# Performance work log

Measured on AMD Instinct MI355X. Metric: run time of the kernel, lower is better.

Reference implementation:

```python
import jax, jax.numpy as jnp
import numpy as np

B, L, D_MODEL, D_INNER, P = 4, 16384, 256, 512, 64  # P = d_state, conj_sym=False
STEP_RESCALE = 1.0


def setup_inputs() -> dict:
    key = jax.random.key(0)
    ks = jax.random.split(key, 11)
    # projections (bias=False)
    W_in = jax.random.normal(ks[0], (D_MODEL, 2 * D_INNER), jnp.float32) * (1.0 / np.sqrt(D_MODEL))
    W_out = jax.random.normal(ks[1], (D_INNER, D_MODEL), jnp.float32) * (1.0 / np.sqrt(D_INNER))
    # diagonal SSM params: Lambda = A_real + i*A_imag, HiPPO-like (negative real part)
    A_real = -0.5 * jnp.ones((P,), jnp.float32) - jax.random.uniform(ks[2], (P,), jnp.float32)
    A_imag = jnp.pi * jnp.arange(P, dtype=jnp.float32) * (jax.random.uniform(ks[3], (P,), jnp.float32) * 0.1 + 0.95)
    B_re = jax.random.normal(ks[4], (P, D_INNER), jnp.float32) * (1.0 / np.sqrt(P))
    B_im = jax.random.normal(ks[5], (P, D_INNER), jnp.float32) * (1.0 / np.sqrt(P))
    C_re = jax.random.normal(ks[6], (D_INNER, P), jnp.float32) * (1.0 / np.sqrt(D_INNER))
    C_im = jax.random.normal(ks[7], (D_INNER, P), jnp.float32) * (1.0 / np.sqrt(D_INNER))
    D = jax.random.normal(ks[8], (D_INNER,), jnp.float32)
    # dt ~ loguniform[dt_min, dt_max]; inv_dt = softplus^{-1}(dt) = dt + log(-expm1(-dt))
    dt = jnp.exp(jax.random.uniform(ks[9], (P,), jnp.float32) * (np.log(0.1) - np.log(0.001)) + np.log(0.001))
    dt = jnp.clip(dt, 1e-4, None)
    inv_dt = dt + jnp.log(-jnp.expm1(-dt))
    x = jax.random.normal(ks[10], (B, L, D_MODEL), jnp.float32)
    return {"x": x, "W_in": W_in, "W_out": W_out, "A_real": A_real, "A_imag": A_imag,
            "B_re": B_re, "B_im": B_im, "C_re": C_re, "C_im": C_im, "D": D, "inv_dt": inv_dt}


def _binop(e1, e2):
    a1, b1 = e1
    a2, b2 = e2
    return a2 * a1, a2 * b1 + b2


def reference(x, W_in, W_out, A_real, A_imag, B_re, B_im, C_re, C_im, D, inv_dt):
    # in_proj + gate split
    x_and_res = x @ W_in                       # (b, l, 2*d_inner)
    u, res = jnp.split(x_and_res, 2, axis=-1)
    u = jax.nn.silu(u)                         # (b, l, d_inner)
    # bilinear discretization of diagonal SSM
    A = A_real + 1j * A_imag                   # (P,)
    dt = STEP_RESCALE * jax.nn.softplus(inv_dt)  # (P,)
    BL = 1.0 / (1.0 - (dt / 2.0) * A)
    dA = BL * (1.0 + (dt / 2.0) * A)           # (P,)
    dB = (BL * dt)[:, None] * (B_re + 1j * B_im)  # (P, d_inner)
    # drive: Bu_t = dB @ u_t
    Bu = u.astype(dA.dtype) @ dB.T             # (b, l, P) complex
    # parallel (associative) scan of h_t = dA*h_{t-1} + Bu_t  (h_0 = 0)
    elems = (jnp.broadcast_to(dA, Bu.shape), Bu)
    _, h = jax.lax.associative_scan(_binop, elems, axis=1)  # (b, l, P)
    C = C_re + 1j * C_im                       # (d_inner, P)
    y = jnp.real(h @ C.T) + D * u              # (b, l, d_inner), + skip D*u
    y = y * jax.nn.silu(res)
    return y @ W_out                           # (b, l, d_model)
```

## Files before the change

kernel.cpp:

```cpp
#include <hip/hip_runtime.h>
#include <math.h>

#define NTOK 65536
#define LSEQ 16384
#define GCH 64
#define NCH 256

typedef __attribute__((ext_vector_type(8))) short short8v;
typedef __attribute__((ext_vector_type(4))) float f32x4;
typedef unsigned short u16;

__device__ __forceinline__ u16 f2bf(float f) {
  unsigned u = __float_as_uint(f);
  return (u16)((u + 0x7FFFu + ((u >> 16) & 1u)) >> 16);
}
__device__ __forceinline__ float bf2f(u16 b) {
  return __uint_as_float(((unsigned)b) << 16);
}
__device__ __forceinline__ unsigned cvtpk_bf16(float lo, float hi) {
  unsigned r;
  asm("v_cvt_pk_bf16_f32 %0, %1, %2" : "=v"(r) : "v"(lo), "v"(hi));
  return r;
}
__device__ __forceinline__ float silu_f(float v) {
  return v * __builtin_amdgcn_rcpf(1.f + __expf(-v));
}
__device__ __forceinline__ void gld16(const u16* g, u16* l) {
  __builtin_amdgcn_global_load_lds((const __attribute__((address_space(1))) void*)g,
                                   (__attribute__((address_space(3))) void*)l, 16, 0, 0);
}

#define GLOAD(dst, ptr) \
  asm volatile("global_load_dwordx4 %0, %1, off" : "=&v"(dst) : "v"(ptr) : "memory")
#define SCHEDB __builtin_amdgcn_sched_barrier(0)
#define WAITV4 asm volatile("s_waitcnt vmcnt(4)" ::: "memory")
#define WAITV1a asm volatile("s_waitcnt vmcnt(1)" ::: "memory")
#define WAITV3L asm volatile("s_waitcnt vmcnt(3) lgkmcnt(0)" ::: "memory")
#define WAITV2 asm volatile("s_waitcnt vmcnt(2) lgkmcnt(0)" ::: "memory")
#define WAITV1 asm volatile("s_waitcnt vmcnt(1) lgkmcnt(0)" ::: "memory")
#define WAITV0 asm volatile("s_waitcnt vmcnt(0) lgkmcnt(0)" ::: "memory")
#define BARRAW asm volatile("s_barrier" ::: "memory")

__global__ void setup_scalar_k(const float* __restrict__ A_real, const float* __restrict__ A_imag,
                               const float* __restrict__ inv_dt,
                               float2* __restrict__ dAf, float2* __restrict__ fvec,
                               float2* __restrict__ powt) {
  int p = threadIdx.x;
  if (p >= 64) return;
  double ar = (double)A_real[p], ai = (double)A_imag[p];
  double dt = log1p(exp((double)inv_dt[p]));
  double zr = 0.5 * dt * ar, zi = 0.5 * dt * ai;
  double d1r = 1.0 - zr;
  double den = d1r * d1r + zi * zi;
  double blr = d1r / den, bli = zi / den;
  double nr = 1.0 + zr, ni = zi;
  double dar = blr * nr - bli * ni;
  double dai = blr * ni + bli * nr;
  dAf[p] = make_float2((float)dar, (float)dai);
  fvec[p] = make_float2((float)(blr * dt), (float)(bli * dt));
  double cr = 1.0, ci = 0.0;
  for (int k = 0; k <= GCH; ++k) {
    powt[p * (GCH + 1) + k] = make_float2((float)cr, (float)ci);
    double t = cr * dar - ci * dai;
    ci = cr * dai + ci * dar;
    cr = t;
  }
}

__global__ void setup_tables_k(const float* __restrict__ B_re, const float* __restrict__ B_im,
                               const float* __restrict__ C_re, const float* __restrict__ C_im,
                               const float* __restrict__ W_in, const float* __restrict__ W_out,
                               const float2* __restrict__ fvec,
                               u16* __restrict__ WinT, u16* __restrict__ dBn,
                               u16* __restrict__ Ccb, u16* __restrict__ WoutT) {
  int idx = blockIdx.x * blockDim.x + threadIdx.x;
  int stride = gridDim.x * blockDim.x;
  for (int i = idx; i < 1024 * 256; i += stride) {
    int n = i >> 8, k = i & 255;
    WinT[i] = f2bf(W_in[k * 1024 + n]);
  }
  for (int i = idx; i < 128 * 512; i += stride) {
    int p = i >> 9, d = i & 511;
    float2 f = fvec[p & 63];
    float br = B_re[(p & 63) * 512 + d], bi = B_im[(p & 63) * 512 + d];
    float v = (p < 64) ? (f.x * br - f.y * bi) : (f.x * bi + f.y * br);
    dBn[i] = f2bf(v);
  }
  for (int i = idx; i < 512 * 128; i += stride) {
    int d = i >> 7, k = i & 127;
    float v = (k < 64) ? C_re[d * 64 + k] : -C_im[d * 64 + (k - 64)];
    Ccb[i] = f2bf(v);
  }
  for (int i = idx; i < 256 * 512; i += stride) {
    int n = i >> 9, k = i & 511;
    WoutT[i] = f2bf(W_out[k * 256 + n]);
  }
}

__global__ __launch_bounds__(512) void k1_fused(
    const float* __restrict__ X, const u16* __restrict__ WinT,
    u16* __restrict__ u_bf, u16* __restrict__ sr_bf) {
  constexpr int KDIM = 256, NT = 8;
  __shared__ u16 As[2][128 * 32];
  __shared__ u16 Bs[3][128 * 32];
  const int tid = threadIdx.x;
  const int w = tid >> 6, l = tid & 63;
  const int wm = w >> 2, wn = w & 3;

  const int lin = blockIdx.x;
  const int cpx = gridDim.x >> 3;
  const int swz = (lin & 7) * cpx + (lin >> 3);
  const int n0 = (swz & 7) * 128;
  const int m0 = (swz >> 3) * 128;

  f32x4 acc[4][2] = {};
  const int fr = l & 15;
  const int kgs = (((l >> 4) ^ (l >> 1)) & 3) * 8;
  const int sr = l >> 2;
  const int scl = l & 3;
  const int scs = scl ^ ((l >> 3) & 3);
  const int arow = w * 16 + sr;
  const float* gA = X + (size_t)(m0 + arow) * KDIM + scl * 8;
  const u16* gB = WinT + (size_t)(n0 + w * 16 + sr) * KDIM + scs * 8;

  float4 rp0, rp1, rq0, rq1;

  auto writeA = [&](int buf, const float4& a0, const float4& a1) {
    unsigned q0 = cvtpk_bf16(a0.x, a0.y), q1 = cvtpk_bf16(a0.z, a0.w);
    unsigned q2 = cvtpk_bf16(a1.x, a1.y), q3 = cvtpk_bf16(a1.z, a1.w);
    *(uint4*)&As[buf][arow * 32 + scs * 8] = make_uint4(q0, q1, q2, q3);
  };
  auto stageB = [&](int buf, int t) { gld16(gB + t * 32, &Bs[buf][w * 512]); };
  auto compute = [&](int ab, int bb) {
    short8v af[4], bfr[2];
#pragma unroll
    for (int mi = 0; mi < 4; ++mi)
      af[mi] = *(const short8v*)&As[ab][(wm * 64 + mi * 16 + fr) * 32 + kgs];
#pragma unroll
    for (int ni = 0; ni < 2; ++ni)
      bfr[ni] = *(const short8v*)&Bs[bb][(wn * 32 + ni * 16 + fr) * 32 + kgs];
#pragma unroll
    for (int mi = 0; mi < 4; ++mi)
#pragma unroll
      for (int ni = 0; ni < 2; ++ni)
        acc[mi][ni] = __builtin_amdgcn_mfma_f32_16x16x32_bf16(af[mi], bfr[ni], acc[mi][ni], 0, 0, 0);
  };

  GLOAD(rp0, gA);          GLOAD(rp1, gA + 4);
  stageB(0, 0);
  GLOAD(rq0, gA + 32);     GLOAD(rq1, gA + 36);
  stageB(1, 1);
  WAITV4; SCHEDB;
  writeA(0, rp0, rp1);
  WAITV3L;
  BARRAW;

#pragma unroll
  for (int t = 0; t < NT; ++t) {
    if (t + 2 < NT) {
      if ((t & 1) == 0) { GLOAD(rp0, gA + (t + 2) * 32); GLOAD(rp1, gA + (t + 2) * 32 + 4); }
      else              { GLOAD(rq0, gA + (t + 2) * 32); GLOAD(rq1, gA + (t + 2) * 32 + 4); }
      stageB((t + 2) % 3, t + 2);
    }
    compute(t & 1, t % 3);
    if (t + 1 < NT) {
      if (t + 2 < NT) { WAITV4; } else { WAITV1a; }
      SCHEDB;
      if (((t + 1) & 1) == 0) writeA(0, rp0, rp1);
      else                    writeA(1, rq0, rq1);
      if (t + 2 < NT) { WAITV3L; } else { WAITV0; }
      BARRAW;
    }
  }

  const int rbase = (l >> 4) * 4;
#pragma unroll
  for (int mi = 0; mi < 4; ++mi) {
#pragma unroll
    for (int ni = 0; ni < 2; ++ni) {
      int gr0 = m0 + wm * 64 + mi * 16 + rbase;
      int gc = n0 + wn * 32 + ni * 16 + fr;
      float s0 = silu_f(acc[mi][ni][0]);
      float s1 = silu_f(acc[mi][ni][1]);
      float s2 = silu_f(acc[mi][ni][2]);
      float s3 = silu_f(acc[mi][ni][3]);
      unsigned p01 = cvtpk_bf16(s0, s1);
      unsigned p23 = cvtpk_bf16(s2, s3);
      u16* Cw = (n0 < 512) ? u_bf : sr_bf;
      int col = gc - ((n0 < 512) ? 0 : 512);
      Cw[(size_t)(gr0 + 0) * 512 + col] = (u16)p01;
      Cw[(size_t)(gr0 + 1) * 512 + col] = (u16)(p01 >> 16);
      Cw[(size_t)(gr0 + 2) * 512 + col] = (u16)p23;
      Cw[(size_t)(gr0 + 3) * 512 + col] = (u16)(p23 >> 16);
    }
  }
}

template<int MODE, int LOG_NBX, int KDIM>
__global__ __launch_bounds__(1024) void mgemm2(
    const u16* __restrict__ Ain, const u16* __restrict__ Bt,
    void* __restrict__ C0, void* __restrict__ C1,
    const float* __restrict__ Dvec) {
  constexpr int NT = KDIM / 32;
  __shared__ u16 As[3][128 * 32];
  __shared__ u16 Bs[3][256 * 32];
  const int tid = threadIdx.x;
  const int w = tid >> 6, l = tid & 63;
  const int wm = w >> 3, wn = w & 7;
  const bool isA = (w < 8);

  const int lin = blockIdx.x;
  const int cpx = gridDim.x >> 3;
  const int swz = (lin & 7) * cpx + (lin >> 3);
  const int n0 = (swz & ((1 << LOG_NBX) - 1)) * 256;
  const int m0 = (swz >> LOG_NBX) * 128;

  f32x4 acc[4][2] = {};

  const int fr = l & 15;
  const int kgs = (((l >> 4) ^ (l >> 1)) & 3) * 8;
  const int sr = l >> 2;
  const int scs = (l & 3) ^ ((l >> 3) & 3);

  const u16* gA = nullptr;
  const u16* gB = nullptr;
  if (isA) gA = Ain + (size_t)(m0 + w * 16 + sr) * KDIM + scs * 8;
  else     gB = Bt + (size_t)(n0 + (w - 8) * 16 + sr) * KDIM + scs * 8;

  auto stage = [&](int buf, int k0) {
    if (isA) {
      gld16(gA + k0, &As[buf][w * 512]);
    } else {
      gld16(gB + k0, &Bs[buf][(w - 8) * 512]);
      gld16(gB + k0 + (size_t)128 * KDIM, &Bs[buf][(w - 8) * 512 + 4096]);
    }
  };
  auto compute = [&](int buf) {
    short8v af[4], bfr[2];
#pragma unroll
    for (int mi = 0; mi < 4; ++mi)
      af[mi] = *(const short8v*)&As[buf][(wm * 64 + mi * 16 + fr) * 32 + kgs];
#pragma unroll
    for (int ni = 0; ni < 2; ++ni)
      bfr[ni] = *(const short8v*)&Bs[buf][(wn * 32 + ni * 16 + fr) * 32 + kgs];
#pragma unroll
    for (int mi = 0; mi < 4; ++mi)
#pragma unroll
      for (int ni = 0; ni < 2; ++ni)
        acc[mi][ni] = __builtin_amdgcn_mfma_f32_16x16x32_bf16(af[mi], bfr[ni], acc[mi][ni], 0, 0, 0);
  };

  stage(0, 0);
  stage(1, 32);
#pragma unroll
  for (int t = 0; t < NT; ++t) {
    if (t + 1 < NT) { if (isA) { WAITV1; } else { WAITV2; } } else { WAITV0; }
    BARRAW;
    if (t + 2 < NT) stage((t + 2) % 3, (t + 2) * 32);
    compute(t % 3);
  }

  const int rbase = (l >> 4) * 4;
#pragma unroll
  for (int mi = 0; mi < 4; ++mi) {
#pragma unroll
    for (int ni = 0; ni < 2; ++ni) {
      int gr0 = m0 + wm * 64 + mi * 16 + rbase;
      int gc = n0 + wn * 32 + ni * 16 + fr;
      if (MODE == 2) {
        float g[4];
#pragma unroll
        for (int j = 0; j < 4; ++j) {
          size_t r = (size_t)(gr0 + j);
          float uu = bf2f(((const u16*)C0)[r * 512 + gc]);
          float sr2 = bf2f(((const u16*)C1)[r * 512 + gc]);
          g[j] = (acc[mi][ni][j] + Dvec[gc] * uu) * sr2;
        }
        unsigned p01 = cvtpk_bf16(g[0], g[1]);
        unsigned p23 = cvtpk_bf16(g[2], g[3]);
        ((u16*)C1)[(size_t)(gr0 + 0) * 512 + gc] = (u16)p01;
        ((u16*)C1)[(size_t)(gr0 + 1) * 512 + gc] = (u16)(p01 >> 16);
        ((u16*)C1)[(size_t)(gr0 + 2) * 512 + gc] = (u16)p23;
        ((u16*)C1)[(size_t)(gr0 + 3) * 512 + gc] = (u16)(p23 >> 16);
      } else {
#pragma unroll
        for (int j = 0; j < 4; ++j)
          ((float*)C0)[(size_t)(gr0 + j) * 256 + gc] = acc[mi][ni][j];
      }
    }
  }
}

__global__ __launch_bounds__(512) void k2_bu_carry(
    const u16* __restrict__ A, const u16* __restrict__ Bt,
    float* __restrict__ Bu, float* __restrict__ carr, float* __restrict__ carr2,
    const float2* __restrict__ dAf, const float2* __restrict__ powt) {
  constexpr int KDIM = 512;
  constexpr int NT = KDIM / 32;
  __shared__ u16 As[3][128 * 32];
  __shared__ u16 Bs[3][128 * 32];
  const int tid = threadIdx.x;
  const int w = tid >> 6, l = tid & 63;
  const int wm = w >> 2, wn = w & 3;

  const int lin = blockIdx.x;
  const int cpx = gridDim.x >> 3;
  const int swz = (lin & 7) * cpx + (lin >> 3);
  const int m0 = swz * 128;

  f32x4 acc[4][2] = {};

  const int lr = l >> 2;
  const int sc = (l & 3) ^ ((l >> 3) & 3);
  const u16* gA = A + (size_t)(m0 + w * 16 + lr) * KDIM + sc * 8;
  const u16* gB = Bt + (size_t)(w * 16 + lr) * KDIM + sc * 8;

  const int fr = l & 15;
  const int kgs = (((l >> 4) ^ (l >> 1)) & 3) * 8;

  auto stage = [&](int buf, int k0) {
    gld16(gA + k0, &As[buf][w * 512]);
    gld16(gB + k0, &Bs[buf][w * 512]);
  };
  auto compute = [&](int buf) {
    short8v af[4], bfr[2];
#pragma unroll
    for (int mi = 0; mi < 4; ++mi)
      af[mi] = *(const short8v*)&As[buf][(wm * 64 + mi * 16 + fr) * 32 + kgs];
#pragma unroll
    for (int ni = 0; ni < 2; ++ni)
      bfr[ni] = *(const short8v*)&Bs[buf][(wn * 32 + ni * 16 + fr) * 32 + kgs];
#pragma unroll
    for (int mi = 0; mi < 4; ++mi)
#pragma unroll
      for (int ni = 0; ni < 2; ++ni)
        acc[mi][ni] = __builtin_amdgcn_mfma_f32_16x16x32_bf16(af[mi], bfr[ni], acc[mi][ni], 0, 0, 0);
  };

  stage(0, 0);
  stage(1, 32);
#pragma unroll
  for (int t = 0; t < NT; ++t) {
    if (t + 1 < NT) { WAITV2; } else { WAITV0; }
    BARRAW;
    if (t + 2 < NT) stage((t + 2) % 3, (t + 2) * 32);
    compute(t % 3);
  }

  const int lg = l >> 4;
  const int rbase = lg * 4;
#pragma unroll
  for (int mi = 0; mi < 4; ++mi)
#pragma unroll
    for (int ni = 0; ni < 2; ++ni) {
      int gr0 = m0 + wm * 64 + mi * 16 + rbase;
      int gc = wn * 32 + ni * 16 + fr;
#pragma unroll
      for (int j = 0; j < 4; ++j)
        Bu[(size_t)(gr0 + j) * 128 + gc] = acc[mi][ni][j];
    }
  const int cu = (m0 >> 6) + wm;
#pragma unroll
  for (int ni = 0; ni < 2; ++ni) {
    int gc = wn * 32 + ni * 16 + fr;
    int p = gc & 63;
    float2 dA = dAf[p];
    float sre = 0.f, sim = 0.f;
#pragma unroll
    for (int mi = 0; mi < 4; ++mi) {
      float tr = 0.f, ti = 0.f;
#pragma unroll
      for (int j = 0; j < 4; ++j) {
        float v = acc[mi][ni][j];
        float nr = fmaf(dA.x, tr, fmaf(-dA.y, ti, v));
        float nim = fmaf(dA.x, ti, dA.y * tr);
        tr = nr; ti = nim;
      }
      float2 wg = powt[p * (GCH + 1) + 60 - lg * 4 - 16 * mi];
      sre = fmaf(wg.x, tr, fmaf(-wg.y, ti, sre));
      sim = fmaf(wg.x, ti, fmaf(wg.y, tr, sim));
    }
    sre += __shfl_xor(sre, 16); sim += __shfl_xor(sim, 16);
    sre += __shfl_xor(sre, 32); sim += __shfl_xor(sim, 32);
    if (lg == 0) {
      size_t crow = (size_t)cu * 128;
      if (gc < 64) { carr[crow + p] = sre;  carr[crow + 64 + p] = sim; }
      else         { carr2[crow + p] = -sim; carr2[crow + 64 + p] = sre; }
    }
  }
}

__global__ void scan_carry_k(const float* __restrict__ carr, const float* __restrict__ carr2,
                             float* __restrict__ offc, const float2* __restrict__ powt) {
  int b = threadIdx.x >> 6;
  int p = threadIdx.x & 63;
  float2 dAG = powt[p * (GCH + 1) + GCH];
  float rr = 0.f, ri = 0.f;
  for (int c0 = 0; c0 < NCH; c0 += 8) {
    float er[8], ei[8];
#pragma unroll
    for (int j = 0; j < 8; ++j) {
      size_t crow = (size_t)(b * NCH + c0 + j) * 128;
      er[j] = carr[crow + p] + carr2[crow + p];
      ei[j] = carr[crow + 64 + p] + carr2[crow + 64 + p];
    }
#pragma unroll
    for (int j = 0; j < 8; ++j) {
      size_t orow = (size_t)(b * NCH + c0 + j) * 128;
      offc[orow + p] = rr;
      offc[orow + 64 + p] = ri;
      float nr = fmaf(dAG.x, rr, fmaf(-dAG.y, ri, er[j]));
      float ni = fmaf(dAG.x, ri, fmaf(dAG.y, rr, ei[j]));
      rr = nr; ri = ni;
    }
  }
}

__global__ __launch_bounds__(256) void scan_emit_k(const float* __restrict__ Bu,
                                                   const float* __restrict__ offc,
                                                   u16* __restrict__ hb,
                                                   const float2* __restrict__ dAf) {
  int unit = blockIdx.x * 4 + (threadIdx.x >> 6);
  int p = threadIdx.x & 63;
  int b = unit >> 8, c = unit & 255;
  float2 dA = dAf[p];
  size_t base = ((size_t)b * LSEQ + (size_t)c * GCH) * 128;
  float hr = offc[(size_t)unit * 128 + p];
  float hi = offc[(size_t)unit * 128 + 64 + p];
  for (int i0 = 0; i0 < GCH; i0 += 8) {
    float br[8], bi[8];
#pragma unroll
    for (int j = 0; j < 8; ++j) {
      br[j] = Bu[base + (size_t)(i0 + j) * 128 + p];
      bi[j] = Bu[base + (size_t)(i0 + j) * 128 + 64 + p];
    }
#pragma unroll
    for (int j = 0; j < 8; ++j) {
      float nr = fmaf(dA.x, hr, fmaf(-dA.y, hi, br[j]));
      float ni = fmaf(dA.x, hi, fmaf(dA.y, hr, bi[j]));
      hr = nr; hi = ni;
      hb[base + (size_t)(i0 + j) * 128 + p] = f2bf(hr);
      hb[base + (size_t)(i0 + j) * 128 + 64 + p] = f2bf(hi);
    }
  }
}

extern "C" void kernel_launch(void* const* d_in, const int* in_sizes, int n_in,
                              void* d_out, int out_size, void* d_ws, size_t ws_size,
                              hipStream_t stream) {
  const float* x      = (const float*)d_in[0];
  const float* W_in   = (const float*)d_in[1];
  const float* W_out  = (const float*)d_in[2];
  const float* A_real = (const float*)d_in[3];
  const float* A_imag = (const float*)d_in[4];
  const float* B_re   = (const float*)d_in[5];
  const float* B_im   = (const float*)d_in[6];
  const float* C_re   = (const float*)d_in[7];
  const float* C_im   = (const float*)d_in[8];
  const float* Dv     = (const float*)d_in[9];
  const float* inv_dt = (const float*)d_in[10];

  u16* u_bf  = (u16*)d_ws;
  u16* sr_bf = u_bf + (size_t)NTOK * 512;
  u16* h_bf  = sr_bf + (size_t)NTOK * 512;
  u16* WinT  = h_bf + (size_t)NTOK * 128;
  u16* dBn   = WinT + 1024 * 256;
  u16* Ccb   = dBn + 128 * 512;
  u16* WoutT = Ccb + 512 * 128;

  float* O    = (float*)d_out;
  float* Bu   = O;
  float* offc = O + 8388608;
  float* carr = O + 8519680;
  float* car2 = O + 8650752;
  float2* powt = (float2*)(O + 8781824);
  float2* dAf  = (float2*)(O + 8790144);
  float2* fvec = (float2*)(O + 8790272);

  setup_scalar_k<<<1, 64, 0, stream>>>(A_real, A_imag, inv_dt, dAf, fvec, powt);
  setup_tables_k<<<256, 256, 0, stream>>>(B_re, B_im, C_re, C_im, W_in, W_out, fvec,
                                          WinT, dBn, Ccb, WoutT);

  k1_fused<<<4096, 512, 0, stream>>>(x, WinT, u_bf, sr_bf);
  k2_bu_carry<<<512, 512, 0, stream>>>(u_bf, dBn, Bu, carr, car2, dAf, powt);
  scan_carry_k<<<1, 256, 0, stream>>>(carr, car2, offc, powt);
  scan_emit_k<<<256, 256, 0, stream>>>(Bu, offc, h_bf, dAf);
  mgemm2<2, 1, 128><<<1024, 1024, 0, stream>>>(h_bf, Ccb, u_bf, sr_bf, Dv);
  mgemm2<3, 0, 512><<<512, 1024, 0, stream>>>(sr_bf, WoutT, O, nullptr, nullptr);
}
```

Before: 223.7 us.

## Pre-convert x to bf16 and stage both GEMM operands via direct LDS loads

Adds a separate pass that converts x to bf16 in workspace, so the in-projection GEMM can load both A and B tiles with global_load_lds into triple-buffered LDS. This replaces the register-staged fp32 loads and in-kernel conversion. The cost is an extra kernel launch plus a write and re-read of a 32 MB bf16 copy of x, traded for a simpler, deeper pipeline. The carry scan kernel also double-buffers its loads, issuing the next 8 chunks before stepping the current ones.

```diff
diff --git a/kernel.cpp b/kernel.cpp
--- a/kernel.cpp
+++ b/kernel.cpp
@@ -30,12 +30,6 @@
                                    (__attribute__((address_space(3))) void*)l, 16, 0, 0);
 }
 
-#define GLOAD(dst, ptr) \
-  asm volatile("global_load_dwordx4 %0, %1, off" : "=&v"(dst) : "v"(ptr) : "memory")
-#define SCHEDB __builtin_amdgcn_sched_barrier(0)
-#define WAITV4 asm volatile("s_waitcnt vmcnt(4)" ::: "memory")
-#define WAITV1a asm volatile("s_waitcnt vmcnt(1)" ::: "memory")
-#define WAITV3L asm volatile("s_waitcnt vmcnt(3) lgkmcnt(0)" ::: "memory")
 #define WAITV2 asm volatile("s_waitcnt vmcnt(2) lgkmcnt(0)" ::: "memory")
 #define WAITV1 asm volatile("s_waitcnt vmcnt(1) lgkmcnt(0)" ::: "memory")
 #define WAITV0 asm volatile("s_waitcnt vmcnt(0) lgkmcnt(0)" ::: "memory")
@@ -97,11 +91,23 @@
   }
 }
 
-__global__ __launch_bounds__(512) void k1_fused(
-    const float* __restrict__ X, const u16* __restrict__ WinT,
+__global__ __launch_bounds__(256) void cvt_x_k(const float* __restrict__ x, u16* __restrict__ xb) {
+  size_t i = ((size_t)blockIdx.x * blockDim.x + threadIdx.x) * 4;
+  size_t stride = (size_t)gridDim.x * blockDim.x * 4;
+  const size_t total = (size_t)NTOK * 256;
+  for (; i < total; i += stride) {
+    float4 v = *(const float4*)(x + i);
+    ushort4 o;
+    o.x = f2bf(v.x); o.y = f2bf(v.y); o.z = f2bf(v.z); o.w = f2bf(v.w);
+    *(ushort4*)(xb + i) = o;
+  }
+}
+
+__global__ __launch_bounds__(512) void k1_gemm(
+    const u16* __restrict__ A, const u16* __restrict__ Bt,
     u16* __restrict__ u_bf, u16* __restrict__ sr_bf) {
   constexpr int KDIM = 256, NT = 8;
-  __shared__ u16 As[2][128 * 32];
+  __shared__ u16 As[3][128 * 32];
   __shared__ u16 Bs[3][128 * 32];
   const int tid = threadIdx.x;
   const int w = tid >> 6, l = tid & 63;
@@ -114,31 +120,27 @@
   const int m0 = (swz >> 3) * 128;
 
   f32x4 acc[4][2] = {};
+
+  const int lr = l >> 2;
+  const int sc = (l & 3) ^ ((l >> 3) & 3);
+  const u16* gA = A + (size_t)(m0 + w * 16 + lr) * KDIM + sc * 8;
+  const u16* gB = Bt + (size_t)(n0 + w * 16 + lr) * KDIM + sc * 8;
+
   const int fr = l & 15;
   const int kgs = (((l >> 4) ^ (l >> 1)) & 3) * 8;
-  const int sr = l >> 2;
-  const int scl = l & 3;
-  const int scs = scl ^ ((l >> 3) & 3);
-  const int arow = w * 16 + sr;
-  const float* gA = X + (size_t)(m0 + arow) * KDIM + scl * 8;
-  const u16* gB = WinT + (size_t)(n0 + w * 16 + sr) * KDIM + scs * 8;
-
-  float4 rp0, rp1, rq0, rq1;
-
-  auto writeA = [&](int buf, const float4& a0, const float4& a1) {
-    unsigned q0 = cvtpk_bf16(a0.x, a0.y), q1 = cvtpk_bf16(a0.z, a0.w);
-    unsigned q2 = cvtpk_bf16(a1.x, a1.y), q3 = cvtpk_bf16(a1.z, a1.w);
-    *(uint4*)&As[buf][arow * 32 + scs * 8] = make_uint4(q0, q1, q2, q3);
-  };
-  auto stageB = [&](int buf, int t) { gld16(gB + t * 32, &Bs[buf][w * 512]); };
-  auto compute = [&](int ab, int bb) {
+
+  auto stage = [&](int buf, int k0) {
+    gld16(gA + k0, &As[buf][w * 512]);
+    gld16(gB + k0, &Bs[buf][w * 512]);
+  };
+  auto compute = [&](int buf) {
     short8v af[4], bfr[2];
 #pragma unroll
     for (int mi = 0; mi < 4; ++mi)
-      af[mi] = *(const short8v*)&As[ab][(wm * 64 + mi * 16 + fr) * 32 + kgs];
+      af[mi] = *(const short8v*)&As[buf][(wm * 64 + mi * 16 + fr) * 32 + kgs];
 #pragma unroll
     for (int ni = 0; ni < 2; ++ni)
-      bfr[ni] = *(const short8v*)&Bs[bb][(wn * 32 + ni * 16 + fr) * 32 + kgs];
+      bfr[ni] = *(const short8v*)&Bs[buf][(wn * 32 + ni * 16 + fr) * 32 + kgs];
 #pragma unroll
     for (int mi = 0; mi < 4; ++mi)
 #pragma unroll
@@ -146,48 +148,31 @@
         acc[mi][ni] = __builtin_amdgcn_mfma_f32_16x16x32_bf16(af[mi], bfr[ni], acc[mi][ni], 0, 0, 0);
   };
 
-  GLOAD(rp0, gA);          GLOAD(rp1, gA + 4);
-  stageB(0, 0);
-  GLOAD(rq0, gA + 32);     GLOAD(rq1, gA + 36);
-  stageB(1, 1);
-  WAITV4; SCHEDB;
-  writeA(0, rp0, rp1);
-  WAITV3L;
-  BARRAW;
-
+  stage(0, 0);
+  stage(1, 32);
 #pragma unroll
   for (int t = 0; t < NT; ++t) {
-    if (t + 2 < NT) {
-      if ((t & 1) == 0) { GLOAD(rp0, gA + (t + 2) * 32); GLOAD(rp1, gA + (t + 2) * 32 + 4); }
-      else              { GLOAD(rq0, gA + (t + 2) * 32); GLOAD(rq1, gA + (t + 2) * 32 + 4); }
-      stageB((t + 2) % 3, t + 2);
-    }
-    compute(t & 1, t % 3);
-    if (t + 1 < NT) {
-      if (t + 2 < NT) { WAITV4; } else { WAITV1a; }
-      SCHEDB;
-      if (((t + 1) & 1) == 0) writeA(0, rp0, rp1);
-      else                    writeA(1, rq0, rq1);
-      if (t + 2 < NT) { WAITV3L; } else { WAITV0; }
-      BARRAW;
-    }
+    if (t + 1 < NT) { WAITV2; } else { WAITV0; }
+    BARRAW;
+    if (t + 2 < NT) stage((t + 2) % 3, (t + 2) * 32);
+    compute(t % 3);
   }
 
   const int rbase = (l >> 4) * 4;
+  u16* Cw = (n0 < 512) ? u_bf : sr_bf;
+  const int cb = (n0 < 512) ? n0 : (n0 - 512);
 #pragma unroll
   for (int mi = 0; mi < 4; ++mi) {
 #pragma unroll
     for (int ni = 0; ni < 2; ++ni) {
       int gr0 = m0 + wm * 64 + mi * 16 + rbase;
-      int gc = n0 + wn * 32 + ni * 16 + fr;
+      int col = cb + wn * 32 + ni * 16 + fr;
       float s0 = silu_f(acc[mi][ni][0]);
       float s1 = silu_f(acc[mi][ni][1]);
       float s2 = silu_f(acc[mi][ni][2]);
       float s3 = silu_f(acc[mi][ni][3]);
       unsigned p01 = cvtpk_bf16(s0, s1);
       unsigned p23 = cvtpk_bf16(s2, s3);
-      u16* Cw = (n0 < 512) ? u_bf : sr_bf;
-      int col = gc - ((n0 < 512) ? 0 : 512);
       Cw[(size_t)(gr0 + 0) * 512 + col] = (u16)p01;
       Cw[(size_t)(gr0 + 1) * 512 + col] = (u16)(p01 >> 16);
       Cw[(size_t)(gr0 + 2) * 512 + col] = (u16)p23;
@@ -396,24 +381,38 @@
   int p = threadIdx.x & 63;
   float2 dAG = powt[p * (GCH + 1) + GCH];
   float rr = 0.f, ri = 0.f;
-  for (int c0 = 0; c0 < NCH; c0 += 8) {
-    float er[8], ei[8];
-#pragma unroll
-    for (int j = 0; j < 8; ++j) {
-      size_t crow = (size_t)(b * NCH + c0 + j) * 128;
-      er[j] = carr[crow + p] + carr2[crow + p];
-      ei[j] = carr[crow + 64 + p] + carr2[crow + 64 + p];
-    }
-#pragma unroll
-    for (int j = 0; j < 8; ++j) {
-      size_t orow = (size_t)(b * NCH + c0 + j) * 128;
-      offc[orow + p] = rr;
-      offc[orow + 64 + p] = ri;
-      float nr = fmaf(dAG.x, rr, fmaf(-dAG.y, ri, er[j]));
-      float ni = fmaf(dAG.x, ri, fmaf(dAG.y, rr, ei[j]));
-      rr = nr; ri = ni;
-    }
-  }
+  float a0[8], b0[8], c0a[8], d0a[8];
+  float a1[8], b1[8], c1a[8], d1a[8];
+
+#define LOADB(cb, A_, B_, C_, D_)                                      \
+  {                                                                     \
+    _Pragma("unroll") for (int j = 0; j < 8; ++j) {                     \
+      size_t crow = (size_t)(b * NCH + (cb) + j) * 128;                 \
+      A_[j] = carr[crow + p]; B_[j] = carr[crow + 64 + p];              \
+      C_[j] = carr2[crow + p]; D_[j] = carr2[crow + 64 + p];            \
+    }                                                                   \
+  }
+#define STEPB(cb, A_, B_, C_, D_)                                      \
+  {                                                                     \
+    _Pragma("unroll") for (int j = 0; j < 8; ++j) {                     \
+      size_t orow = (size_t)(b * NCH + (cb) + j) * 128;                 \
+      offc[orow + p] = rr; offc[orow + 64 + p] = ri;                    \
+      float er = A_[j] + C_[j], ei = B_[j] + D_[j];                     \
+      float nr = fmaf(dAG.x, rr, fmaf(-dAG.y, ri, er));                 \
+      float ni = fmaf(dAG.x, ri, fmaf(dAG.y, rr, ei));                  \
+      rr = nr; ri = ni;                                                 \
+    }                                                                   \
+  }
+
+  LOADB(0, a0, b0, c0a, d0a);
+  for (int c0 = 0; c0 < NCH; c0 += 16) {
+    LOADB(c0 + 8, a1, b1, c1a, d1a);
+    STEPB(c0, a0, b0, c0a, d0a);
+    if (c0 + 16 < NCH) LOADB(c0 + 16, a0, b0, c0a, d0a);
+    STEPB(c0 + 8, a1, b1, c1a, d1a);
+  }
+#undef LOADB
+#undef STEPB
 }
 
 __global__ __launch_bounds__(256) void scan_emit_k(const float* __restrict__ Bu,
@@ -460,7 +459,8 @@
   const float* Dv     = (const float*)d_in[9];
   const float* inv_dt = (const float*)d_in[10];
 
-  u16* u_bf  = (u16*)d_ws;
+  u16* xb    = (u16*)d_ws;
+  u16* u_bf  = xb + (size_t)NTOK * 256;
   u16* sr_bf = u_bf + (size_t)NTOK * 512;
   u16* h_bf  = sr_bf + (size_t)NTOK * 512;
   u16* WinT  = h_bf + (size_t)NTOK * 128;
@@ -480,8 +480,9 @@
   setup_scalar_k<<<1, 64, 0, stream>>>(A_real, A_imag, inv_dt, dAf, fvec, powt);
   setup_tables_k<<<256, 256, 0, stream>>>(B_re, B_im, C_re, C_im, W_in, W_out, fvec,
                                           WinT, dBn, Ccb, WoutT);
-
-  k1_fused<<<4096, 512, 0, stream>>>(x, WinT, u_bf, sr_bf);
+  cvt_x_k<<<2048, 256, 0, stream>>>(x, xb);
+
+  k1_gemm<<<4096, 512, 0, stream>>>(xb, WinT, u_bf, sr_bf);
   k2_bu_carry<<<512, 512, 0, stream>>>(u_bf, dBn, Bu, carr, car2, dAf, powt);
   scan_carry_k<<<1, 256, 0, stream>>>(carr, car2, offc, powt);
   scan_emit_k<<<256, 256, 0, stream>>>(Bu, offc, h_bf, dAf);
```

Measured after the change: 210.6 us. 1.06x faster.
